# Performance work log

Measured on AMD Instinct MI355X. Metric: run time of the kernel, lower is better.

## Reference

```python
import jax, jax.numpy as jnp
from jax import lax
import numpy as np

B, C, H, W = 32, 256, 16, 16          # batch, planes, feature-map HxW
NBUF, REPS, LAB = 100000, 256, 10     # buffer size, reps dim, label dim
D = REPS + LAB                        # retrieval_data feature dim
DH = 64                               # cross_dim_head (heads=1 -> inner=64)
INNER = DH
EPS = 1e-5


def _ln(x, g, b):
    m = x.mean(-1, keepdims=True)
    v = ((x - m) ** 2).mean(-1, keepdims=True)
    return (x - m) * lax.rsqrt(v + EPS) * g + b


def _conv(x, w):
    return lax.conv_general_dilated(x, w, (1, 1), 'SAME',
                                    dimension_numbers=('NCHW', 'OIHW', 'NCHW'))


def _forward(x, conv1_w, conv2_w, bn1_g, bn1_b, bn2_g, bn2_b, retrieval_data,
             ln_attn_g, ln_attn_b, ln_ctx_g, ln_ctx_b, wq, wk, wv, wqe, wo, bo,
             ln_ff_g, ln_ff_b, w1, b1, w2, b2, topk):
    # eval-mode BatchNorm with running mean=0, var=1
    bn = lambda y, g, b: y * g[None, :, None, None] + b[None, :, None, None]
    out = jax.nn.relu(bn(_conv(x, conv1_w), bn1_g, bn1_b))
    out = bn(_conv(out, conv2_w), bn2_g, bn2_b)
    out = jax.nn.relu(out + x)                        # identity shortcut
    t = out.reshape(B, C, H * W).transpose(0, 2, 1)   # [B, n, C] tokens

    # ---- retrieval cross-attention (PreNorm on x and on context) ----
    xn = _ln(t, ln_attn_g, ln_attn_b)
    ctx = _ln(retrieval_data, ln_ctx_g, ln_ctx_b)     # [NBUF, D]
    q = xn @ wq                                        # [B, n, INNER]
    emb = q @ wqe                                      # [B, n, REPS]
    e0 = emb[:, 0, :]                                  # original loop only uses position 0
    buf_reps = ctx[:, :REPS]                           # [NBUF, REPS]
    # squared L2 has the same ordering as the L2 norm used by torch.topk(largest=False)
    dist2 = jnp.sum((buf_reps[None] - e0[:, None]) ** 2, axis=-1)  # [B, NBUF]
    idx = lax.top_k(-dist2, topk)[1]                   # [B, topk] nearest indices
    retrieved = jnp.take(ctx, idx, axis=0)             # [B, topk, D]; identical for all n positions
    reps_r, labels_r = retrieved[..., :REPS], retrieved[..., REPS:]
    k = reps_r @ wk                                    # reps_for_k: K from reps  [B, topk, INNER]
    v = labels_r @ wv                                  # V from labels            [B, topk, INNER]
    sim = jnp.einsum('bnd,bjd->bnj', q, k) * DH ** -0.5
    attn = jax.nn.softmax(sim, axis=-1)
    o = jnp.einsum('bnj,bjd->bnd', attn, v)
    t = o @ wo + bo + t

    # ---- feed-forward (PreNorm, GEGLU, mult=1) ----
    h = _ln(t, ln_ff_g, ln_ff_b) @ w1 + b1             # [B, n, 2C]
    a, g = jnp.split(h, 2, axis=-1)
    t = (a * jax.nn.gelu(g, approximate=False)) @ w2 + b2 + t

    return t.transpose(0, 2, 1).reshape(B, C, H, W)


def setup_inputs() -> dict:
    key = jax.random.key(0)
    ks = jax.random.split(key, 12)
    s = 0.02
    return {
        'x': jax.random.normal(ks[0], (B, C, H, W), jnp.float32),
        'conv1_w': jax.random.normal(ks[1], (C, C, 3, 3), jnp.float32) * s,
        'conv2_w': jax.random.normal(ks[2], (C, C, 3, 3), jnp.float32) * s,
        'bn1_g': jnp.ones((C,), jnp.float32), 'bn1_b': jnp.zeros((C,), jnp.float32),
        'bn2_g': jnp.ones((C,), jnp.float32), 'bn2_b': jnp.zeros((C,), jnp.float32),
        'retrieval_data': jax.random.normal(ks[3], (NBUF, D), jnp.float32),
        'ln_attn_g': jnp.ones((C,), jnp.float32), 'ln_attn_b': jnp.zeros((C,), jnp.float32),
        'ln_ctx_g': jnp.ones((D,), jnp.float32), 'ln_ctx_b': jnp.zeros((D,), jnp.float32),
        'wq': jax.random.normal(ks[4], (C, INNER), jnp.float32) * s,
        'wk': jax.random.normal(ks[5], (REPS, INNER), jnp.float32) * s,
        'wv': jax.random.normal(ks[6], (LAB, INNER), jnp.float32) * s,
        'wqe': jax.random.normal(ks[7], (INNER, REPS), jnp.float32) * s,
        'wo': jax.random.normal(ks[8], (INNER, C), jnp.float32) * s,
        'bo': jnp.zeros((C,), jnp.float32),
        'ln_ff_g': jnp.ones((C,), jnp.float32), 'ln_ff_b': jnp.zeros((C,), jnp.float32),
        'w1': jax.random.normal(ks[9], (C, 2 * C), jnp.float32) * s,
        'b1': jnp.zeros((2 * C,), jnp.float32),
        'w2': jax.random.normal(ks[10], (C, C), jnp.float32) * s,
        'b2': jnp.zeros((C,), jnp.float32),
        'topk': 32,
    }


def reference(x, conv1_w, conv2_w, bn1_g, bn1_b, bn2_g, bn2_b, retrieval_data,
              ln_attn_g, ln_attn_b, ln_ctx_g, ln_ctx_b, wq, wk, wv, wqe, wo, bo,
              ln_ff_g, ln_ff_b, w1, b1, w2, b2, topk):
    return _forward(x, conv1_w, conv2_w, bn1_g, bn1_b, bn2_g, bn2_b, retrieval_data,
                    ln_attn_g, ln_attn_b, ln_ctx_g, ln_ctx_b, wq, wk, wv, wqe, wo, bo,
                    ln_ff_g, ln_ff_b, w1, b1, w2, b2, topk)
```

## Files before the change

### kernel.cpp

```cpp
#include <hip/hip_runtime.h>
#include <hip/hip_bf16.h>
#include <math.h>

#define DEV __device__ __forceinline__

typedef __attribute__((ext_vector_type(8))) short bf16x8;
typedef __attribute__((ext_vector_type(4))) float f32x4;
typedef __attribute__((ext_vector_type(4))) unsigned int u32x4;
typedef __attribute__((ext_vector_type(2))) unsigned int u32x2;

DEV float b2f(unsigned int u) { return __uint_as_float(u << 16); }
DEV unsigned short f2b(float f) {
    unsigned int x = __float_as_uint(f);
    unsigned int r = x + 0x7fffu + ((x >> 16) & 1u);
    return (unsigned short)(r >> 16);
}
DEV unsigned int pack2(float a, float b) {
    return (unsigned int)f2b(a) | ((unsigned int)f2b(b) << 16);
}
DEV float gelu_exact(float g) {
    return 0.5f * g * (1.f + erff(g * 0.70710678118654752f));
}

constexpr size_t WP1  = 0;
constexpr size_t WP2  = WP1  + 1179648;
constexpr size_t BPQ  = WP2  + 1179648;
constexpr size_t BPO  = BPQ  + 32768;
constexpr size_t BP1  = BPO  + 32768;
constexpr size_t BP2  = BP1  + 262144;
constexpr size_t XTP  = BP2  + 131072;
constexpr size_t O1P  = XTP  + 5308416;
constexpr size_t TBUF = O1P  + 5308416;
constexpr size_t QB   = TBUF + 8388608;
constexpr size_t E0P  = QB   + 1048576;
constexpr size_t DIST = E0P  + 16384;
constexpr size_t CANDV= DIST + 12800000;
constexpr size_t CANDI= CANDV+ 262144;
constexpr size_t IDXB = CANDI+ 262144;
constexpr size_t KBF  = IDXB + 4096;
constexpr size_t VBF  = KBF  + 262144;
constexpr size_t OBF  = VBF  + 262144;
constexpr size_t T2B  = OBF  + 1048576;
constexpr size_t XN2  = T2B  + 8388608;
constexpr size_t UBF  = XN2  + 4194304;

__global__ __launch_bounds__(256) void setup_k(
    const float* __restrict__ x, const float* __restrict__ c1w, const float* __restrict__ c2w,
    const float* __restrict__ wq, const float* __restrict__ wo,
    const float* __restrict__ w1, const float* __restrict__ w2,
    unsigned short* __restrict__ wp1, unsigned short* __restrict__ wp2,
    unsigned short* __restrict__ pq, unsigned short* __restrict__ po,
    unsigned short* __restrict__ p1, unsigned short* __restrict__ p2,
    unsigned short* __restrict__ xtp, unsigned short* __restrict__ o1p)
{
    int blk = blockIdx.x, tid = threadIdx.x;
    if (blk < 576) {
        const float* src = (blk < 288) ? c1w : c2w;
        unsigned short* dst = (blk < 288) ? wp1 : wp2;
        int f = (blk % 288) * 256 + tid;
        int lane = f & 63, s = f >> 6;
        int t = s >> 7, rem = s & 127, kc = rem >> 4, ntg = rem & 15;
        int co = ntg * 16 + (lane & 15);
        int ci0 = kc * 32 + ((lane >> 4) << 3);
        unsigned short v[8];
#pragma unroll
        for (int j = 0; j < 8; ++j) v[j] = f2b(src[((size_t)co * 256 + ci0 + j) * 9 + t]);
        u32x4 q;
        q.x = (unsigned)v[0] | ((unsigned)v[1] << 16);
        q.y = (unsigned)v[2] | ((unsigned)v[3] << 16);
        q.z = (unsigned)v[4] | ((unsigned)v[5] << 16);
        q.w = (unsigned)v[6] | ((unsigned)v[7] << 16);
        *(u32x4*)(dst + (size_t)f * 8) = q;
    } else if (blk < 688) {
        int f = (blk - 576) * 256 + tid;
        const float* src; unsigned short* dst; int NTT, lf;
        if (f < 2048)       { src = wq; dst = pq; NTT = 4;  lf = f; }
        else if (f < 4096)  { src = wo; dst = po; NTT = 16; lf = f - 2048; }
        else if (f < 20480) { src = w1; dst = p1; NTT = 32; lf = f - 4096; }
        else                { src = w2; dst = p2; NTT = 16; lf = f - 20480; }
        int lane = lf & 63, s = lf >> 6;
        int kc = s / NTT, ntg = s % NTT;
        int N = NTT * 16;
        int k0 = kc * 32 + ((lane >> 4) << 3), n = ntg * 16 + (lane & 15);
        unsigned short v[8];
#pragma unroll
        for (int j = 0; j < 8; ++j) v[j] = f2b(src[(size_t)(k0 + j) * N + n]);
        u32x4 q;
        q.x = (unsigned)v[0] | ((unsigned)v[1] << 16);
        q.y = (unsigned)v[2] | ((unsigned)v[3] << 16);
        q.z = (unsigned)v[4] | ((unsigned)v[5] << 16);
        q.w = (unsigned)v[6] | ((unsigned)v[7] << 16);
        *(u32x4*)(dst + (size_t)lf * 8) = q;
    } else {
        int t = blk - 688;
        int img = t >> 3, cc = t & 7;
        int h = tid >> 4, w = tid & 15;
        unsigned short* dst = xtp + ((size_t)img * 324 + (h + 1) * 18 + (w + 1)) * 256 + cc * 32;
        const float* src = x + (size_t)img * 65536 + (size_t)cc * 32 * 256 + tid;
        unsigned short v[32];
#pragma unroll
        for (int j = 0; j < 32; ++j) v[j] = f2b(src[j * 256]);
        u32x4* dp = (u32x4*)dst;
#pragma unroll
        for (int i = 0; i < 4; ++i) {
            u32x4 q;
            q.x = (unsigned)v[i*8+0] | ((unsigned)v[i*8+1] << 16);
            q.y = (unsigned)v[i*8+2] | ((unsigned)v[i*8+3] << 16);
            q.z = (unsigned)v[i*8+4] | ((unsigned)v[i*8+5] << 16);
            q.w = (unsigned)v[i*8+6] | ((unsigned)v[i*8+7] << 16);
            dp[i] = q;
        }
        for (int cell = tid; cell < 324; cell += 256) {
            int hh = cell / 18, ww = cell - hh * 18;
            if (hh == 0 || hh == 17 || ww == 0 || ww == 17) {
                u32x4 z = (u32x4)0u;
                u32x4* zp1 = (u32x4*)(xtp + ((size_t)img * 324 + cell) * 256 + cc * 32);
                u32x4* zp2 = (u32x4*)(o1p + ((size_t)img * 324 + cell) * 256 + cc * 32);
#pragma unroll
                for (int i = 0; i < 4; ++i) { zp1[i] = z; zp2[i] = z; }
            }
        }
    }
}

template<int EPI>
__global__ __launch_bounds__(256, 2) void conv_mfma(const unsigned short* __restrict__ Asrc,
                                                    const unsigned short* __restrict__ wpack,
                                                    const float* __restrict__ bng,
                                                    const float* __restrict__ bnb,
                                                    const unsigned short* __restrict__ resid,
                                                    unsigned short* __restrict__ outP,
                                                    float* __restrict__ outT)
{
    __shared__ __align__(16) float part[4][4][4][64][4];
    int blk = blockIdx.x;
    int img = blk >> 4, rem = blk & 15;
    int mo = rem >> 2, nq = rem & 3;
    int tid = threadIdx.x;
    int wv = tid >> 6, lane = tid & 63;
    int lq = lane >> 4, lr = lane & 15;
    int m0 = mo * 64;
    int n0 = nq * 64;

    f32x4 acc[4][4];
#pragma unroll
    for (int i = 0; i < 4; ++i)
#pragma unroll
        for (int j = 0; j < 4; ++j) acc[i][j] = 0.f;

    int abase[4];
#pragma unroll
    for (int mt = 0; mt < 4; ++mt) {
        int m = m0 + mt * 16 + lr;
        int h = m >> 4, w = m & 15;
        abase[mt] = (img * 324 + (h + 1) * 18 + (w + 1)) * 256 + lq * 8;
    }
    int bb0 = (n0 >> 4) * 512 + lane * 8;

    for (int kc2 = 0; kc2 < 2; ++kc2) {
        int kc = wv * 2 + kc2;
#pragma unroll
        for (int tap = 0; tap < 9; ++tap) {
            int dh = tap / 3 - 1, dw = tap % 3 - 1;
            int aoff = (dh * 18 + dw) * 256 + kc * 32;
            bf16x8 a[4], b[4];
#pragma unroll
            for (int mt = 0; mt < 4; ++mt) a[mt] = *(const bf16x8*)(Asrc + abase[mt] + aoff);
            int boff = (tap * 8 + kc) * 8192 + bb0;
#pragma unroll
            for (int nt = 0; nt < 4; ++nt) b[nt] = *(const bf16x8*)(wpack + boff + nt * 512);
#pragma unroll
            for (int mt = 0; mt < 4; ++mt)
#pragma unroll
                for (int nt = 0; nt < 4; ++nt)
                    acc[mt][nt] = __builtin_amdgcn_mfma_f32_16x16x32_bf16(a[mt], b[nt], acc[mt][nt], 0, 0, 0);
        }
    }
#pragma unroll
    for (int mt = 0; mt < 4; ++mt)
#pragma unroll
        for (int nt = 0; nt < 4; ++nt)
            *(f32x4*)&part[wv][mt][nt][lane][0] = acc[mt][nt];
    __syncthreads();
    int mt = wv;
#pragma unroll
    for (int nt = 0; nt < 4; ++nt) {
        f32x4 s0 = *(const f32x4*)&part[0][mt][nt][lane][0];
        f32x4 s1 = *(const f32x4*)&part[1][mt][nt][lane][0];
        f32x4 s2 = *(const f32x4*)&part[2][mt][nt][lane][0];
        f32x4 s3 = *(const f32x4*)&part[3][mt][nt][lane][0];
        f32x4 sum;
#pragma unroll
        for (int r = 0; r < 4; ++r) sum[r] = (s0[r] + s1[r]) + (s2[r] + s3[r]);
        int co = n0 + nt * 16 + lr;
        float g = bng[co], bb = bnb[co];
#pragma unroll
        for (int r = 0; r < 4; ++r) {
            int m = m0 + mt * 16 + lq * 4 + r;
            int h = m >> 4, w = m & 15;
            float v = sum[r] * g + bb;
            if (EPI == 0) {
                v = fmaxf(v, 0.f);
                outP[((size_t)img * 324 + (h + 1) * 18 + (w + 1)) * 256 + co] = f2b(v);
            } else {
                v += b2f(resid[((size_t)img * 324 + (h + 1) * 18 + (w + 1)) * 256 + co]);
                v = fmaxf(v, 0.f);
                outT[((size_t)img * 256 + m) * 256 + co] = v;
            }
        }
    }
}

__global__ __launch_bounds__(256) void lnq_k(
    const float* __restrict__ t, const float* __restrict__ g, const float* __restrict__ bta,
    const unsigned short* __restrict__ bpq, const float* __restrict__ wqe,
    unsigned short* __restrict__ qb, unsigned short* __restrict__ e0p)
{
    __shared__ __align__(16) unsigned int frag[64 * 132];
    __shared__ float qrow[64];
    int bx = blockIdx.x, tid = threadIdx.x;
    int wv = tid >> 6, lane = tid & 63;
    int c = lane * 4;
    f32x4 gv = *(const f32x4*)(g + c);
    f32x4 bv = *(const f32x4*)(bta + c);
#pragma unroll
    for (int p = 0; p < 16; ++p) {
        int rl = wv * 16 + p;
        f32x4 x = *(const f32x4*)(t + (size_t)(bx * 64 + rl) * 256 + c);
        float s  = x[0] + x[1] + x[2] + x[3];
        float ss = x[0]*x[0] + x[1]*x[1] + x[2]*x[2] + x[3]*x[3];
#pragma unroll
        for (int off = 32; off >= 1; off >>= 1) { s += __shfl_xor(s, off); ss += __shfl_xor(ss, off); }
        float mean = s * (1.f / 256.f);
        float var  = ss * (1.f / 256.f) - mean * mean;
        float rstd = rsqrtf(fmaxf(var, 0.f) + 1e-5f);
        float y0 = (x[0]-mean)*rstd*gv[0] + bv[0];
        float y1 = (x[1]-mean)*rstd*gv[1] + bv[1];
        float y2 = (x[2]-mean)*rstd*gv[2] + bv[2];
        float y3 = (x[3]-mean)*rstd*gv[3] + bv[3];
        frag[rl * 132 + 2 * lane]     = pack2(y0, y1);
        frag[rl * 132 + 2 * lane + 1] = pack2(y2, y3);
    }
    __syncthreads();
    int lq = lane >> 4, lr = lane & 15;
    f32x4 acc[4];
#pragma unroll
    for (int nt = 0; nt < 4; ++nt) acc[nt] = 0.f;
    const short* sA = (const short*)frag;
#pragma unroll
    for (int kc = 0; kc < 8; ++kc) {
        bf16x8 a = *(const bf16x8*)(sA + (wv * 16 + lr) * 264 + kc * 32 + lq * 8);
#pragma unroll
        for (int nt = 0; nt < 4; ++nt) {
            bf16x8 bfr = *(const bf16x8*)(bpq + (size_t)(kc * 4 + nt) * 512 + lane * 8);
            acc[nt] = __builtin_amdgcn_mfma_f32_16x16x32_bf16(a, bfr, acc[nt], 0, 0, 0);
        }
    }
#pragma unroll
    for (int nt = 0; nt < 4; ++nt)
#pragma unroll
        for (int r = 0; r < 4; ++r)
            qb[(size_t)(bx * 64 + wv * 16 + lq * 4 + r) * 64 + nt * 16 + lr] = f2b(acc[nt][r]);
    if ((bx & 3) == 0 && wv == 0 && lq == 0) {
#pragma unroll
        for (int nt = 0; nt < 4; ++nt) qrow[nt * 16 + lr] = acc[nt][0];
    }
    __syncthreads();
    if ((bx & 3) == 0) {
        int b = bx >> 2;
        int r = tid;
        float a2 = 0.f;
#pragma unroll 8
        for (int d = 0; d < 64; ++d) a2 += qrow[d] * wqe[d * 256 + r];
        int nt = b >> 4, kc = r >> 5;
        int ln_ = (b & 15) + (((r >> 3) & 3) << 4);
        int j = r & 7;
        e0p[(((nt * 8 + kc) * 64) + ln_) * 8 + j] = f2b(a2);
    }
}

__global__ __launch_bounds__(256, 4) void lndist_k(
    const float* __restrict__ ctx, const float* __restrict__ lgam, const float* __restrict__ lbet,
    const unsigned short* __restrict__ e0p, float* __restrict__ dist)
{
    __shared__ __align__(16) unsigned int frag[32 * 132];
    __shared__ __align__(16) float rn2s[32];
    int r0 = blockIdx.x * 32;
    int tid = threadIdx.x;
    int wv = tid >> 6, lane = tid & 63;

    float2 d0[8], d1[8], d2[8];
    const float* base = ctx + (size_t)(r0 + wv * 8) * 266;
#pragma unroll
    for (int p = 0; p < 8; ++p) {
        const float* rowp = base + p * 266;
        d0[p] = *(const float2*)(rowp + 2 * lane);
        d1[p] = *(const float2*)(rowp + 128 + 2 * lane);
        if (lane < 5) d2[p] = *(const float2*)(rowp + 256 + 2 * lane);
        else { d2[p].x = 0.f; d2[p].y = 0.f; }
    }
    float2 g0 = *(const float2*)(lgam + 2 * lane);
    float2 g1 = *(const float2*)(lgam + 128 + 2 * lane);
    float2 b0 = *(const float2*)(lbet + 2 * lane);
    float2 b1 = *(const float2*)(lbet + 128 + 2 * lane);

#pragma unroll
    for (int p = 0; p < 8; ++p) {
        int rl = wv * 8 + p;
        float s  = d0[p].x + d0[p].y + d1[p].x + d1[p].y + d2[p].x + d2[p].y;
        float ss = d0[p].x*d0[p].x + d0[p].y*d0[p].y + d1[p].x*d1[p].x + d1[p].y*d1[p].y
                 + d2[p].x*d2[p].x + d2[p].y*d2[p].y;
#pragma unroll
        for (int off = 32; off >= 1; off >>= 1) { s += __shfl_xor(s, off); ss += __shfl_xor(ss, off); }
        float mean = s * (1.f / 266.f);
        float var  = ss * (1.f / 266.f) - mean * mean;
        float rstd = rsqrtf(fmaxf(var, 0.f) + 1e-5f);
        float c0 = (d0[p].x - mean) * rstd * g0.x + b0.x;
        float c1 = (d0[p].y - mean) * rstd * g0.y + b0.y;
        float c2 = (d1[p].x - mean) * rstd * g1.x + b1.x;
        float c3 = (d1[p].y - mean) * rstd * g1.y + b1.y;
        frag[rl * 132 + lane]      = pack2(c0, c1);
        frag[rl * 132 + 64 + lane] = pack2(c2, c3);
        float nsq = c0*c0 + c1*c1 + c2*c2 + c3*c3;
#pragma unroll
        for (int off = 32; off >= 1; off >>= 1) nsq += __shfl_xor(nsq, off);
        if (lane == 0) rn2s[rl] = nsq;
    }
    __syncthreads();

    int lq = lane >> 4, lr = lane & 15;
    int rt = wv & 1, ch = wv >> 1;
    f32x4 acc = 0.f;
    const short* sA = (const short*)frag;
#pragma unroll
    for (int kc = 0; kc < 8; ++kc) {
        bf16x8 a = *(const bf16x8*)(sA + (rt * 16 + lr) * 264 + kc * 32 + lq * 8);
        bf16x8 b = *(const bf16x8*)(e0p + ((ch * 8 + kc) * 64 + lane) * 8);
        acc = __builtin_amdgcn_mfma_f32_16x16x32_bf16(a, b, acc, 0, 0, 0);
    }
    int mbase = r0 + rt * 16 + lq * 4;
    f32x4 rv = *(f32x4*)(rn2s + rt * 16 + lq * 4);
    f32x4 o;
#pragma unroll
    for (int r = 0; r < 4; ++r) o[r] = rv[r] - 2.f * acc[r];
    *(f32x4*)(dist + (size_t)(ch * 16 + lr) * 100000 + mbase) = o;
}

__global__ __launch_bounds__(256) void topk1w(const float* __restrict__ dist,
                                              float* __restrict__ candv,
                                              int* __restrict__ candi)
{
    __shared__ float sv[6400];
    int c = blockIdx.x, b = blockIdx.y;
    int tid = threadIdx.x;
    int wv = tid >> 6, lane = tid & 63;
    const float* src = dist + (size_t)b * 100000 + c * 6250;
    for (int i = tid; i < 6250; i += 256) sv[i] = src[i];
    for (int i = 6250 + tid; i < 6400; i += 256) sv[i] = 3e38f;
    __syncthreads();
    int base = wv * 1600;
    float* cvp = candv + (((size_t)b * 16 + c) * 4 + wv) * 32;
    int*   cip = candi + (((size_t)b * 16 + c) * 4 + wv) * 32;
    for (int it = 0; it < 32; ++it) {
        float lm = 3e38f; int li = base;
#pragma unroll
        for (int t = 0; t < 25; ++t) {
            int i = base + lane + t * 64;
            float v = sv[i];
            if (v < lm) { lm = v; li = i; }
        }
#pragma unroll
        for (int off = 32; off >= 1; off >>= 1) {
            float ov = __shfl_xor(lm, off);
            int oi = __shfl_xor(li, off);
            if (ov < lm) { lm = ov; li = oi; }
        }
        if (lane == 0) {
            cvp[it] = lm;
            cip[it] = c * 6250 + li;
            sv[li] = 3e38f;
        }
        __builtin_amdgcn_wave_barrier();
    }
}

__global__ __launch_bounds__(256) void selkv_k(const float* __restrict__ candv,
                                               const int* __restrict__ candi,
                                               const float* __restrict__ ctx,
                                               const float* __restrict__ g,
                                               const float* __restrict__ bta,
                                               const float* __restrict__ wk,
                                               const float* __restrict__ wvm,
                                               float* __restrict__ kb,
                                               float* __restrict__ vb)
{
    __shared__ float sv[2048]; __shared__ int si[2048];
    __shared__ float fv[128];  __shared__ int fi[128];
    __shared__ int rows[32];
    __shared__ float cnv[32][268];
    int b = blockIdx.x, tid = threadIdx.x;
    int wv = tid >> 6, lane = tid & 63;
    for (int i = tid; i < 2048; i += 256) {
        sv[i] = candv[(size_t)b * 2048 + i];
        si[i] = candi[(size_t)b * 2048 + i];
    }
    __syncthreads();
    {
        int base = wv * 512;
        for (int it = 0; it < 32; ++it) {
            float lm = 3e38f; int li = base;
#pragma unroll
            for (int t = 0; t < 8; ++t) {
                int i = base + lane + t * 64;
                float v = sv[i];
                if (v < lm) { lm = v; li = i; }
            }
#pragma unroll
            for (int off = 32; off >= 1; off >>= 1) {
                float ov = __shfl_xor(lm, off);
                int oi = __shfl_xor(li, off);
                if (ov < lm) { lm = ov; li = oi; }
            }
            if (lane == 0) { fv[wv * 32 + it] = lm; fi[wv * 32 + it] = si[li]; sv[li] = 3e38f; }
            __builtin_amdgcn_wave_barrier();
        }
    }
    __syncthreads();
    if (wv == 0) {
        for (int it = 0; it < 32; ++it) {
            float lm = 3e38f; int li = 0;
#pragma unroll
            for (int t = 0; t < 2; ++t) {
                int i = lane + t * 64;
                float v = fv[i];
                if (v < lm) { lm = v; li = i; }
            }
#pragma unroll
            for (int off = 32; off >= 1; off >>= 1) {
                float ov = __shfl_xor(lm, off);
                int oi = __shfl_xor(li, off);
                if (ov < lm) { lm = ov; li = oi; }
            }
            if (lane == 0) { rows[it] = fi[li]; fv[li] = 3e38f; }
            __builtin_amdgcn_wave_barrier();
        }
    }
    __syncthreads();
    for (int p = 0; p < 8; ++p) {
        int j = wv * 8 + p;
        int rrow = rows[j];
        const float* pp = ctx + (size_t)rrow * 266;
        float2 a0 = *(const float2*)(pp + 2 * lane);
        float2 a1 = *(const float2*)(pp + 128 + 2 * lane);
        float x4 = 0.f, x5 = 0.f;
        if (lane < 5) { float2 a2 = *(const float2*)(pp + 256 + 2 * lane); x4 = a2.x; x5 = a2.y; }
        float s  = a0.x + a0.y + a1.x + a1.y + x4 + x5;
        float ss = a0.x*a0.x + a0.y*a0.y + a1.x*a1.x + a1.y*a1.y + x4*x4 + x5*x5;
#pragma unroll
        for (int off = 32; off >= 1; off >>= 1) { s += __shfl_xor(s, off); ss += __shfl_xor(ss, off); }
        float mean = s * (1.f / 266.f);
        float var  = ss * (1.f / 266.f) - mean * mean;
        float rstd = rsqrtf(fmaxf(var, 0.f) + 1e-5f);
        float2 g0 = *(const float2*)(g + 2 * lane);
        float2 g1 = *(const float2*)(g + 128 + 2 * lane);
        float2 b0 = *(const float2*)(bta + 2 * lane);
        float2 b1 = *(const float2*)(bta + 128 + 2 * lane);
        cnv[j][2*lane]       = (a0.x - mean) * rstd * g0.x + b0.x;
        cnv[j][2*lane + 1]   = (a0.y - mean) * rstd * g0.y + b0.y;
        cnv[j][128 + 2*lane] = (a1.x - mean) * rstd * g1.x + b1.x;
        cnv[j][129 + 2*lane] = (a1.y - mean) * rstd * g1.y + b1.y;
        if (lane < 5) {
            float2 g2 = *(const float2*)(g + 256 + 2 * lane);
            float2 b2 = *(const float2*)(bta + 256 + 2 * lane);
            cnv[j][256 + 2*lane] = (x4 - mean) * rstd * g2.x + b2.x;
            cnv[j][257 + 2*lane] = (x5 - mean) * rstd * g2.y + b2.y;
        }
    }
    __syncthreads();
    {
        float acc[8];
#pragma unroll
        for (int p = 0; p < 8; ++p) acc[p] = 0.f;
        int j0 = wv * 8;
        for (int r = 0; r < 256; r += 4) {
            float w0 = wk[(r + 0) * 64 + lane];
            float w1_ = wk[(r + 1) * 64 + lane];
            float w2_ = wk[(r + 2) * 64 + lane];
            float w3 = wk[(r + 3) * 64 + lane];
#pragma unroll
            for (int p = 0; p < 8; ++p) {
                f32x4 cv = *(const f32x4*)&cnv[j0 + p][r];
                acc[p] += cv[0] * w0 + cv[1] * w1_ + cv[2] * w2_ + cv[3] * w3;
            }
        }
#pragma unroll
        for (int p = 0; p < 8; ++p)
            kb[((size_t)b * 32 + j0 + p) * 64 + lane] = acc[p];
#pragma unroll
        for (int p = 0; p < 8; ++p) {
            float a2 = 0.f;
#pragma unroll
            for (int r = 0; r < 10; ++r) a2 += cnv[j0 + p][256 + r] * wvm[r * 64 + lane];
            vb[((size_t)b * 32 + j0 + p) * 64 + lane] = a2;
        }
    }
}

__global__ __launch_bounds__(256) void attn_k(const unsigned short* __restrict__ q,
                                              const float* __restrict__ kb,
                                              const float* __restrict__ vb,
                                              unsigned short* __restrict__ ob)
{
    __shared__ float kl[32 * 66];
    __shared__ float vl[32 * 66];
    __shared__ float ql[8 * 64];
    __shared__ float pl[8 * 32];
    int b = blockIdx.x >> 5, pxg = blockIdx.x & 31;
    int px_base = pxg * 8;
    int tid = threadIdx.x;

    for (int i = tid; i < 2048; i += 256) {
        int row = i >> 6, d = i & 63;
        kl[row * 66 + d] = kb[(size_t)b * 2048 + i];
        vl[row * 66 + d] = vb[(size_t)b * 2048 + i];
    }
    for (int i = tid; i < 512; i += 256) {
        ql[i] = b2f(q[((size_t)b * 256 + px_base) * 64 + i]);
    }
    __syncthreads();

    int wv = tid >> 6, lane = tid & 63;
    int lp = wv * 2 + (lane >> 5);
    int j = lane & 31;

    const float* qp = ql + lp * 64;
    const float* kp = kl + j * 66;
    float s = 0.f;
#pragma unroll
    for (int d = 0; d < 64; ++d) s += qp[d] * kp[d];
    s *= 0.125f;

    float mx = s;
#pragma unroll
    for (int off = 16; off >= 1; off >>= 1) mx = fmaxf(mx, __shfl_xor(mx, off));
    float p = expf(s - mx);
    float sum = p;
#pragma unroll
    for (int off = 16; off >= 1; off >>= 1) sum += __shfl_xor(sum, off);
    p /= sum;
    pl[lp * 32 + j] = p;

    int d0 = 2 * j;
    float o0 = 0.f, o1 = 0.f;
#pragma unroll
    for (int jj = 0; jj < 32; ++jj) {
        float pj = pl[lp * 32 + jj];
        float2 vv = *(const float2*)(vl + jj * 66 + d0);
        o0 += pj * vv.x;
        o1 += pj * vv.y;
    }
    ((unsigned int*)ob)[(((size_t)b * 256 + px_base + lp) * 64 + d0) >> 1] = pack2(o0, o1);
}

__global__ __launch_bounds__(256) void tail_k(
    const unsigned short* __restrict__ A,
    const unsigned short* __restrict__ Bpo,
    const float* __restrict__ bo, const float* __restrict__ tres,
    const float* __restrict__ lng, const float* __restrict__ lnb,
    const unsigned short* __restrict__ Bp1, const float* __restrict__ b1,
    const unsigned short* __restrict__ Bp2, const float* __restrict__ b2,
    float* __restrict__ out)
{
    __shared__ __align__(16) float tile[32 * 268];
    __shared__ __align__(16) unsigned short xt[32 * 264];
    int m0 = blockIdx.x * 32;
    int tid = threadIdx.x, wv = tid >> 6, lane = tid & 63, lq = lane >> 4, lr = lane & 15;
    int n0 = wv * 64;
    const short* xts = (const short*)xt;

    {
        f32x4 acc[2][4];
#pragma unroll
        for (int i = 0; i < 2; ++i)
#pragma unroll
            for (int j = 0; j < 4; ++j) acc[i][j] = 0.f;
        const unsigned short* a0p = A + (size_t)(m0 + lr) * 64 + lq * 8;
#pragma unroll
        for (int kc = 0; kc < 2; ++kc) {
            bf16x8 a0 = *(const bf16x8*)(a0p + kc * 32);
            bf16x8 a1 = *(const bf16x8*)(a0p + 16 * 64 + kc * 32);
#pragma unroll
            for (int nt = 0; nt < 4; ++nt) {
                bf16x8 bfr = *(const bf16x8*)(Bpo + (size_t)(kc * 16 + (n0 >> 4) + nt) * 512 + lane * 8);
                acc[0][nt] = __builtin_amdgcn_mfma_f32_16x16x32_bf16(a0, bfr, acc[0][nt], 0, 0, 0);
                acc[1][nt] = __builtin_amdgcn_mfma_f32_16x16x32_bf16(a1, bfr, acc[1][nt], 0, 0, 0);
            }
        }
#pragma unroll
        for (int mt = 0; mt < 2; ++mt)
#pragma unroll
            for (int nt = 0; nt < 4; ++nt)
#pragma unroll
                for (int r = 0; r < 4; ++r)
                    tile[(mt * 16 + lq * 4 + r) * 268 + n0 + nt * 16 + lr] = acc[mt][nt][r];
    }
    __syncthreads();

    {
        int row = tid >> 3, c0 = (tid & 7) * 32;
        const float* trp = tres + (size_t)(m0 + row) * 256 + c0;
        float v[32];
#pragma unroll
        for (int i = 0; i < 8; ++i) {
            f32x4 t4 = *(f32x4*)(tile + row * 268 + c0 + i * 4);
            f32x4 rr = *(const f32x4*)(trp + i * 4);
            f32x4 bb = *(const f32x4*)(bo + c0 + i * 4);
#pragma unroll
            for (int k = 0; k < 4; ++k) v[i*4+k] = t4[k] + rr[k] + bb[k];
        }
#pragma unroll
        for (int i = 0; i < 8; ++i) {
            f32x4 o; o[0] = v[i*4]; o[1] = v[i*4+1]; o[2] = v[i*4+2]; o[3] = v[i*4+3];
            *(f32x4*)(tile + row * 268 + c0 + i * 4) = o;
        }
        float s = 0.f, ss = 0.f;
#pragma unroll
        for (int i = 0; i < 32; ++i) { s += v[i]; ss += v[i] * v[i]; }
#pragma unroll
        for (int off = 1; off <= 4; off <<= 1) { s += __shfl_xor(s, off); ss += __shfl_xor(ss, off); }
        float mean = s * (1.f / 256.f);
        float var  = ss * (1.f / 256.f) - mean * mean;
        float rstd = rsqrtf(fmaxf(var, 0.f) + 1e-5f);
        unsigned int pk[16];
#pragma unroll
        for (int i = 0; i < 16; ++i) {
            float y0 = (v[2*i]   - mean) * rstd * lng[c0+2*i]   + lnb[c0+2*i];
            float y1 = (v[2*i+1] - mean) * rstd * lng[c0+2*i+1] + lnb[c0+2*i+1];
            pk[i] = pack2(y0, y1);
        }
        u32x4* dp = (u32x4*)(xt + row * 264 + c0);
#pragma unroll
        for (int i = 0; i < 4; ++i) {
            u32x4 o; o.x = pk[i*4]; o.y = pk[i*4+1]; o.z = pk[i*4+2]; o.w = pk[i*4+3];
            dp[i] = o;
        }
    }
    __syncthreads();

    f32x4 fa[2][4], fg[2][4];
#pragma unroll
    for (int i = 0; i < 2; ++i)
#pragma unroll
        for (int j = 0; j < 4; ++j) { fa[i][j] = 0.f; fg[i][j] = 0.f; }
#pragma unroll
    for (int kc = 0; kc < 8; ++kc) {
        bf16x8 a0 = *(const bf16x8*)(xts + lr * 264 + kc * 32 + lq * 8);
        bf16x8 a1 = *(const bf16x8*)(xts + (16 + lr) * 264 + kc * 32 + lq * 8);
#pragma unroll
        for (int nt = 0; nt < 4; ++nt) {
            bf16x8 bA = *(const bf16x8*)(Bp1 + (size_t)(kc * 32 + (n0 >> 4) + nt) * 512 + lane * 8);
            bf16x8 bG = *(const bf16x8*)(Bp1 + (size_t)(kc * 32 + 16 + (n0 >> 4) + nt) * 512 + lane * 8);
            fa[0][nt] = __builtin_amdgcn_mfma_f32_16x16x32_bf16(a0, bA, fa[0][nt], 0, 0, 0);
            fa[1][nt] = __builtin_amdgcn_mfma_f32_16x16x32_bf16(a1, bA, fa[1][nt], 0, 0, 0);
            fg[0][nt] = __builtin_amdgcn_mfma_f32_16x16x32_bf16(a0, bG, fg[0][nt], 0, 0, 0);
            fg[1][nt] = __builtin_amdgcn_mfma_f32_16x16x32_bf16(a1, bG, fg[1][nt], 0, 0, 0);
        }
    }
    __syncthreads();
#pragma unroll
    for (int nt = 0; nt < 4; ++nt) {
        int col = n0 + nt * 16 + lr;
        float ba = b1[col], bg = b1[256 + col];
#pragma unroll
        for (int mt = 0; mt < 2; ++mt)
#pragma unroll
            for (int r = 0; r < 4; ++r) {
                float a = fa[mt][nt][r] + ba;
                float gg = fg[mt][nt][r] + bg;
                xt[(mt * 16 + lq * 4 + r) * 264 + col] = f2b(a * gelu_exact(gg));
            }
    }
    __syncthreads();

    {
        f32x4 c2[2][4];
#pragma unroll
        for (int i = 0; i < 2; ++i)
#pragma unroll
            for (int j = 0; j < 4; ++j) c2[i][j] = 0.f;
#pragma unroll
        for (int kc = 0; kc < 8; ++kc) {
            bf16x8 a0 = *(const bf16x8*)(xts + lr * 264 + kc * 32 + lq * 8);
            bf16x8 a1 = *(const bf16x8*)(xts + (16 + lr) * 264 + kc * 32 + lq * 8);
#pragma unroll
            for (int nt = 0; nt < 4; ++nt) {
                bf16x8 bfr = *(const bf16x8*)(Bp2 + (size_t)(kc * 16 + (n0 >> 4) + nt) * 512 + lane * 8);
                c2[0][nt] = __builtin_amdgcn_mfma_f32_16x16x32_bf16(a0, bfr, c2[0][nt], 0, 0, 0);
                c2[1][nt] = __builtin_amdgcn_mfma_f32_16x16x32_bf16(a1, bfr, c2[1][nt], 0, 0, 0);
            }
        }
#pragma unroll
        for (int nt = 0; nt < 4; ++nt) {
            int col = n0 + nt * 16 + lr;
            float bv = b2[col];
#pragma unroll
            for (int mt = 0; mt < 2; ++mt)
#pragma unroll
                for (int r = 0; r < 4; ++r) {
                    int m = mt * 16 + lq * 4 + r;
                    tile[m * 268 + col] = c2[mt][nt][r] + bv + tile[m * 268 + col];
                }
        }
    }
    __syncthreads();

    {
        int b = m0 >> 8, px0 = m0 & 255;
        int c = tid;
        float* dp = out + ((size_t)b * 256 + c) * 256 + px0;
#pragma unroll
        for (int q = 0; q < 8; ++q) {
            f32x4 o;
            o[0] = tile[(q * 4 + 0) * 268 + c];
            o[1] = tile[(q * 4 + 1) * 268 + c];
            o[2] = tile[(q * 4 + 2) * 268 + c];
            o[3] = tile[(q * 4 + 3) * 268 + c];
            *(f32x4*)(dp + q * 4) = o;
        }
    }
}

extern "C" void kernel_launch(void* const* d_in, const int* in_sizes, int n_in,
                              void* d_out, int out_size, void* d_ws, size_t ws_size,
                              hipStream_t stream)
{
    (void)in_sizes; (void)n_in; (void)out_size; (void)ws_size;
    const float* x    = (const float*)d_in[0];
    const float* c1w  = (const float*)d_in[1];
    const float* c2w  = (const float*)d_in[2];
    const float* bn1g = (const float*)d_in[3];
    const float* bn1b = (const float*)d_in[4];
    const float* bn2g = (const float*)d_in[5];
    const float* bn2b = (const float*)d_in[6];
    const float* rdat = (const float*)d_in[7];
    const float* lag  = (const float*)d_in[8];
    const float* labp = (const float*)d_in[9];
    const float* lcg  = (const float*)d_in[10];
    const float* lcb  = (const float*)d_in[11];
    const float* wq   = (const float*)d_in[12];
    const float* wk   = (const float*)d_in[13];
    const float* wv   = (const float*)d_in[14];
    const float* wqe  = (const float*)d_in[15];
    const float* wo   = (const float*)d_in[16];
    const float* bo   = (const float*)d_in[17];
    const float* lfg  = (const float*)d_in[18];
    const float* lfb  = (const float*)d_in[19];
    const float* w1   = (const float*)d_in[20];
    const float* b1   = (const float*)d_in[21];
    const float* w2   = (const float*)d_in[22];
    const float* b2   = (const float*)d_in[23];

    char* ws = (char*)d_ws;
    unsigned short* wp1  = (unsigned short*)(ws + WP1);
    unsigned short* wp2  = (unsigned short*)(ws + WP2);
    unsigned short* bpq  = (unsigned short*)(ws + BPQ);
    unsigned short* bpo  = (unsigned short*)(ws + BPO);
    unsigned short* bp1  = (unsigned short*)(ws + BP1);
    unsigned short* bp2  = (unsigned short*)(ws + BP2);
    unsigned short* xtp  = (unsigned short*)(ws + XTP);
    unsigned short* o1p  = (unsigned short*)(ws + O1P);
    float*          tb   = (float*)(ws + TBUF);
    unsigned short* qb   = (unsigned short*)(ws + QB);
    unsigned short* e0p  = (unsigned short*)(ws + E0P);
    float*          dist = (float*)(ws + DIST);
    float*          cdv  = (float*)(ws + CANDV);
    int*            cdi  = (int*)(ws + CANDI);
    float*          kb   = (float*)(ws + KBF);
    float*          vbuf = (float*)(ws + VBF);
    unsigned short* ob   = (unsigned short*)(ws + OBF);
    float*          outp = (float*)d_out;

    setup_k<<<944, 256, 0, stream>>>(x, c1w, c2w, wq, wo, w1, w2,
                                     wp1, wp2, bpq, bpo, bp1, bp2, xtp, o1p);
    conv_mfma<0><<<512, 256, 0, stream>>>(xtp, wp1, bn1g, bn1b, nullptr, o1p, nullptr);
    conv_mfma<1><<<512, 256, 0, stream>>>(o1p, wp2, bn2g, bn2b, xtp, nullptr, tb);
    lnq_k<<<128, 256, 0, stream>>>(tb, lag, labp, bpq, wqe, qb, e0p);
    lndist_k<<<3125, 256, 0, stream>>>(rdat, lcg, lcb, e0p, dist);
    topk1w<<<dim3(16, 32), 256, 0, stream>>>(dist, cdv, cdi);
    selkv_k<<<32, 256, 0, stream>>>(cdv, cdi, rdat, lcg, lcb, wk, wv, kb, vbuf);
    attn_k<<<1024, 256, 0, stream>>>(qb, kb, vbuf, ob);
    tail_k<<<256, 256, 0, stream>>>(ob, bpo, bo, tb, lfg, lfb, bp1, b1, bp2, b2, outp);
}
```

Baseline: 395.3 us.

## Fuse attention into tail kernel and keep top-k candidates in registers

Removes the separate attention kernel. Each tail block now computes softmax attention for its 32 pixels into shared memory and feeds that result straight into the output-projection MFMA, so the attention output no longer round-trips through global memory and one launch is dropped. The iterative top-k selection in topk1w and selkv_k now holds candidates in per-lane registers and rescans only the winning lane after each pick, instead of rescanning shared memory every iteration. The cost is more register use and longer tail blocks, since 256 blocks now each redo the K/V loads for their batch.

```diff
diff --git a/kernel.cpp b/kernel.cpp
--- a/kernel.cpp
+++ b/kernel.cpp
@@ -40,9 +40,6 @@
 constexpr size_t KBF  = IDXB + 4096;
 constexpr size_t VBF  = KBF  + 262144;
 constexpr size_t OBF  = VBF  + 262144;
-constexpr size_t T2B  = OBF  + 1048576;
-constexpr size_t XN2  = T2B  + 8388608;
-constexpr size_t UBF  = XN2  + 4194304;
 
 __global__ __launch_bounds__(256) void setup_k(
     const float* __restrict__ x, const float* __restrict__ c1w, const float* __restrict__ c2w,
@@ -350,37 +347,43 @@
                                               float* __restrict__ candv,
                                               int* __restrict__ candi)
 {
-    __shared__ float sv[6400];
     int c = blockIdx.x, b = blockIdx.y;
     int tid = threadIdx.x;
     int wv = tid >> 6, lane = tid & 63;
-    const float* src = dist + (size_t)b * 100000 + c * 6250;
-    for (int i = tid; i < 6250; i += 256) sv[i] = src[i];
-    for (int i = 6250 + tid; i < 6400; i += 256) sv[i] = 3e38f;
-    __syncthreads();
     int base = wv * 1600;
+    const float* src = dist + (size_t)b * 100000 + c * 6250 + base;
+    float v[25];
+#pragma unroll
+    for (int t = 0; t < 25; ++t) {
+        int i = lane + t * 64;
+        v[t] = (base + i < 6250) ? src[i] : 3e38f;
+    }
+    float lm = v[0]; int lt = 0;
+#pragma unroll
+    for (int t = 1; t < 25; ++t) if (v[t] < lm) { lm = v[t]; lt = t; }
     float* cvp = candv + (((size_t)b * 16 + c) * 4 + wv) * 32;
     int*   cip = candi + (((size_t)b * 16 + c) * 4 + wv) * 32;
     for (int it = 0; it < 32; ++it) {
-        float lm = 3e38f; int li = base;
-#pragma unroll
-        for (int t = 0; t < 25; ++t) {
-            int i = base + lane + t * 64;
-            float v = sv[i];
-            if (v < lm) { lm = v; li = i; }
-        }
+        float gm = lm;
+        int gmeta = (lane << 5) | lt;
 #pragma unroll
         for (int off = 32; off >= 1; off >>= 1) {
-            float ov = __shfl_xor(lm, off);
-            int oi = __shfl_xor(li, off);
-            if (ov < lm) { lm = ov; li = oi; }
-        }
+            float ov = __shfl_xor(gm, off);
+            int om = __shfl_xor(gmeta, off);
+            if (ov < gm) { gm = ov; gmeta = om; }
+        }
+        int gl = gmeta >> 5, gt = gmeta & 31;
         if (lane == 0) {
-            cvp[it] = lm;
-            cip[it] = c * 6250 + li;
-            sv[li] = 3e38f;
-        }
-        __builtin_amdgcn_wave_barrier();
+            cvp[it] = gm;
+            cip[it] = c * 6250 + base + gl + gt * 64;
+        }
+        if (lane == gl) {
+#pragma unroll
+            for (int t = 0; t < 25; ++t) if (t == gt) v[t] = 3e38f;
+            lm = v[0]; lt = 0;
+#pragma unroll
+            for (int t = 1; t < 25; ++t) if (v[t] < lm) { lm = v[t]; lt = t; }
+        }
     }
 }
 
@@ -394,55 +397,66 @@
                                                float* __restrict__ kb,
                                                float* __restrict__ vb)
 {
-    __shared__ float sv[2048]; __shared__ int si[2048];
     __shared__ float fv[128];  __shared__ int fi[128];
     __shared__ int rows[32];
     __shared__ float cnv[32][268];
     int b = blockIdx.x, tid = threadIdx.x;
     int wv = tid >> 6, lane = tid & 63;
-    for (int i = tid; i < 2048; i += 256) {
-        sv[i] = candv[(size_t)b * 2048 + i];
-        si[i] = candi[(size_t)b * 2048 + i];
-    }
-    __syncthreads();
     {
-        int base = wv * 512;
+        const float* cvb = candv + (size_t)b * 2048 + wv * 512;
+        const int*   cib = candi + (size_t)b * 2048 + wv * 512;
+        float v8[8]; int id8[8];
+#pragma unroll
+        for (int t = 0; t < 8; ++t) { v8[t] = cvb[lane + t * 64]; id8[t] = cib[lane + t * 64]; }
+        float lm = v8[0]; int lt = 0, lid = id8[0];
+#pragma unroll
+        for (int t = 1; t < 8; ++t) if (v8[t] < lm) { lm = v8[t]; lt = t; lid = id8[t]; }
         for (int it = 0; it < 32; ++it) {
-            float lm = 3e38f; int li = base;
-#pragma unroll
-            for (int t = 0; t < 8; ++t) {
-                int i = base + lane + t * 64;
-                float v = sv[i];
-                if (v < lm) { lm = v; li = i; }
-            }
+            float gm = lm; int gid = lid;
+            int gmeta = (lane << 3) | lt;
 #pragma unroll
             for (int off = 32; off >= 1; off >>= 1) {
-                float ov = __shfl_xor(lm, off);
-                int oi = __shfl_xor(li, off);
-                if (ov < lm) { lm = ov; li = oi; }
-            }
-            if (lane == 0) { fv[wv * 32 + it] = lm; fi[wv * 32 + it] = si[li]; sv[li] = 3e38f; }
-            __builtin_amdgcn_wave_barrier();
+                float ov = __shfl_xor(gm, off);
+                int oi = __shfl_xor(gid, off);
+                int om = __shfl_xor(gmeta, off);
+                if (ov < gm) { gm = ov; gid = oi; gmeta = om; }
+            }
+            int gl = gmeta >> 3, gt = gmeta & 7;
+            if (lane == 0) { fv[wv * 32 + it] = gm; fi[wv * 32 + it] = gid; }
+            if (lane == gl) {
+#pragma unroll
+                for (int t = 0; t < 8; ++t) if (t == gt) v8[t] = 3e38f;
+                lm = v8[0]; lt = 0; lid = id8[0];
+#pragma unroll
+                for (int t = 1; t < 8; ++t) if (v8[t] < lm) { lm = v8[t]; lt = t; lid = id8[t]; }
+            }
         }
     }
     __syncthreads();
     if (wv == 0) {
+        float v2[2]; int id2[2];
+#pragma unroll
+        for (int t = 0; t < 2; ++t) { v2[t] = fv[lane + t * 64]; id2[t] = fi[lane + t * 64]; }
+        float lm = v2[0]; int lt = 0, lid = id2[0];
+        if (v2[1] < lm) { lm = v2[1]; lt = 1; lid = id2[1]; }
         for (int it = 0; it < 32; ++it) {
-            float lm = 3e38f; int li = 0;
-#pragma unroll
-            for (int t = 0; t < 2; ++t) {
-                int i = lane + t * 64;
-                float v = fv[i];
-                if (v < lm) { lm = v; li = i; }
-            }
+            float gm = lm; int gid = lid;
+            int gmeta = (lane << 1) | lt;
 #pragma unroll
             for (int off = 32; off >= 1; off >>= 1) {
-                float ov = __shfl_xor(lm, off);
-                int oi = __shfl_xor(li, off);
-                if (ov < lm) { lm = ov; li = oi; }
-            }
-            if (lane == 0) { rows[it] = fi[li]; fv[li] = 3e38f; }
-            __builtin_amdgcn_wave_barrier();
+                float ov = __shfl_xor(gm, off);
+                int oi = __shfl_xor(gid, off);
+                int om = __shfl_xor(gmeta, off);
+                if (ov < gm) { gm = ov; gid = oi; gmeta = om; }
+            }
+            int gl = gmeta >> 1, gt = gmeta & 1;
+            if (lane == 0) rows[it] = gid;
+            if (lane == gl) {
+#pragma unroll
+                for (int t = 0; t < 2; ++t) if (t == gt) v2[t] = 3e38f;
+                lm = v2[0]; lt = 0; lid = id2[0];
+                if (v2[1] < lm) { lm = v2[1]; lt = 1; lid = id2[1]; }
+            }
         }
     }
     __syncthreads();
@@ -506,64 +520,10 @@
     }
 }
 
-__global__ __launch_bounds__(256) void attn_k(const unsigned short* __restrict__ q,
-                                              const float* __restrict__ kb,
-                                              const float* __restrict__ vb,
-                                              unsigned short* __restrict__ ob)
-{
-    __shared__ float kl[32 * 66];
-    __shared__ float vl[32 * 66];
-    __shared__ float ql[8 * 64];
-    __shared__ float pl[8 * 32];
-    int b = blockIdx.x >> 5, pxg = blockIdx.x & 31;
-    int px_base = pxg * 8;
-    int tid = threadIdx.x;
-
-    for (int i = tid; i < 2048; i += 256) {
-        int row = i >> 6, d = i & 63;
-        kl[row * 66 + d] = kb[(size_t)b * 2048 + i];
-        vl[row * 66 + d] = vb[(size_t)b * 2048 + i];
-    }
-    for (int i = tid; i < 512; i += 256) {
-        ql[i] = b2f(q[((size_t)b * 256 + px_base) * 64 + i]);
-    }
-    __syncthreads();
-
-    int wv = tid >> 6, lane = tid & 63;
-    int lp = wv * 2 + (lane >> 5);
-    int j = lane & 31;
-
-    const float* qp = ql + lp * 64;
-    const float* kp = kl + j * 66;
-    float s = 0.f;
-#pragma unroll
-    for (int d = 0; d < 64; ++d) s += qp[d] * kp[d];
-    s *= 0.125f;
-
-    float mx = s;
-#pragma unroll
-    for (int off = 16; off >= 1; off >>= 1) mx = fmaxf(mx, __shfl_xor(mx, off));
-    float p = expf(s - mx);
-    float sum = p;
-#pragma unroll
-    for (int off = 16; off >= 1; off >>= 1) sum += __shfl_xor(sum, off);
-    p /= sum;
-    pl[lp * 32 + j] = p;
-
-    int d0 = 2 * j;
-    float o0 = 0.f, o1 = 0.f;
-#pragma unroll
-    for (int jj = 0; jj < 32; ++jj) {
-        float pj = pl[lp * 32 + jj];
-        float2 vv = *(const float2*)(vl + jj * 66 + d0);
-        o0 += pj * vv.x;
-        o1 += pj * vv.y;
-    }
-    ((unsigned int*)ob)[(((size_t)b * 256 + px_base + lp) * 64 + d0) >> 1] = pack2(o0, o1);
-}
-
 __global__ __launch_bounds__(256) void tail_k(
-    const unsigned short* __restrict__ A,
+    const unsigned short* __restrict__ qg,
+    const float* __restrict__ kbuf,
+    const float* __restrict__ vbuf,
     const unsigned short* __restrict__ Bpo,
     const float* __restrict__ bo, const float* __restrict__ tres,
     const float* __restrict__ lng, const float* __restrict__ lnb,
@@ -577,6 +537,55 @@
     int tid = threadIdx.x, wv = tid >> 6, lane = tid & 63, lq = lane >> 4, lr = lane & 15;
     int n0 = wv * 64;
     const short* xts = (const short*)xt;
+    int b = m0 >> 8, px0 = m0 & 255;
+
+    {
+        float* kl = tile;
+        float* vl = tile + 2112;
+        float* ql = tile + 4224;
+        float* pl = tile + 6272;
+        for (int i = tid; i < 2048; i += 256) {
+            int row = i >> 6, d = i & 63;
+            kl[row * 66 + d] = kbuf[(size_t)b * 2048 + i];
+            vl[row * 66 + d] = vbuf[(size_t)b * 2048 + i];
+        }
+        for (int i = tid; i < 2048; i += 256) {
+            ql[i] = b2f(qg[((size_t)b * 256 + px0) * 64 + i]);
+        }
+        __syncthreads();
+        int lp = wv * 2 + (lane >> 5);
+        int j = lane & 31;
+#pragma unroll
+        for (int pass = 0; pass < 4; ++pass) {
+            int px = pass * 8 + lp;
+            const float* qp = ql + px * 64;
+            const float* kp = kl + j * 66;
+            float s = 0.f;
+#pragma unroll
+            for (int d = 0; d < 64; ++d) s += qp[d] * kp[d];
+            s *= 0.125f;
+            float mx = s;
+#pragma unroll
+            for (int off = 16; off >= 1; off >>= 1) mx = fmaxf(mx, __shfl_xor(mx, off));
+            float p = expf(s - mx);
+            float sum = p;
+#pragma unroll
+            for (int off = 16; off >= 1; off >>= 1) sum += __shfl_xor(sum, off);
+            p /= sum;
+            pl[lp * 32 + j] = p;
+            int d0 = 2 * j;
+            float o0 = 0.f, o1 = 0.f;
+#pragma unroll
+            for (int jj = 0; jj < 32; ++jj) {
+                float pj = pl[lp * 32 + jj];
+                float2 vv = *(const float2*)(vl + jj * 66 + d0);
+                o0 += pj * vv.x;
+                o1 += pj * vv.y;
+            }
+            *(unsigned int*)(xt + px * 264 + d0) = pack2(o0, o1);
+        }
+    }
+    __syncthreads();
 
     {
         f32x4 acc[2][4];
@@ -584,11 +593,10 @@
         for (int i = 0; i < 2; ++i)
 #pragma unroll
             for (int j = 0; j < 4; ++j) acc[i][j] = 0.f;
-        const unsigned short* a0p = A + (size_t)(m0 + lr) * 64 + lq * 8;
 #pragma unroll
         for (int kc = 0; kc < 2; ++kc) {
-            bf16x8 a0 = *(const bf16x8*)(a0p + kc * 32);
-            bf16x8 a1 = *(const bf16x8*)(a0p + 16 * 64 + kc * 32);
+            bf16x8 a0 = *(const bf16x8*)(xts + lr * 264 + kc * 32 + lq * 8);
+            bf16x8 a1 = *(const bf16x8*)(xts + (16 + lr) * 264 + kc * 32 + lq * 8);
 #pragma unroll
             for (int nt = 0; nt < 4; ++nt) {
                 bf16x8 bfr = *(const bf16x8*)(Bpo + (size_t)(kc * 16 + (n0 >> 4) + nt) * 512 + lane * 8);
@@ -596,6 +604,7 @@
                 acc[1][nt] = __builtin_amdgcn_mfma_f32_16x16x32_bf16(a1, bfr, acc[1][nt], 0, 0, 0);
             }
         }
+        __syncthreads();
 #pragma unroll
         for (int mt = 0; mt < 2; ++mt)
 #pragma unroll
@@ -715,7 +724,6 @@
     __syncthreads();
 
     {
-        int b = m0 >> 8, px0 = m0 & 255;
         int c = tid;
         float* dp = out + ((size_t)b * 256 + c) * 256 + px0;
 #pragma unroll
@@ -777,7 +785,6 @@
     int*            cdi  = (int*)(ws + CANDI);
     float*          kb   = (float*)(ws + KBF);
     float*          vbuf = (float*)(ws + VBF);
-    unsigned short* ob   = (unsigned short*)(ws + OBF);
     float*          outp = (float*)d_out;
 
     setup_k<<<944, 256, 0, stream>>>(x, c1w, c2w, wq, wo, w1, w2,
@@ -788,6 +795,5 @@
     lndist_k<<<3125, 256, 0, stream>>>(rdat, lcg, lcb, e0p, dist);
     topk1w<<<dim3(16, 32), 256, 0, stream>>>(dist, cdv, cdi);
     selkv_k<<<32, 256, 0, stream>>>(cdv, cdi, rdat, lcg, lcb, wk, wv, kb, vbuf);
-    attn_k<<<1024, 256, 0, stream>>>(qb, kb, vbuf, ob);
-    tail_k<<<256, 256, 0, stream>>>(ob, bpo, bo, tb, lfg, lfb, bp1, b1, bp2, b2, outp);
-}
+    tail_k<<<256, 256, 0, stream>>>(qb, kb, vbuf, bpo, bo, tb, lfg, lfb, bp1, b1, bp2, b2, outp);
+}
```

Result: no change. 400.9 us (+1.4%).
